# Performance work log

Hardware: AMD Instinct MI355X
Metric: run time of the kernel (lower is better)

Reference implementation:

```python
import jax, jax.numpy as jnp
import numpy as np

N_NODES = 100000
IN_FEATS = 512
H_FEATS = 128
N_HOPS = 3
N_NIE = N_HOPS + 1  # 4 per-hop branches
N_EDGES = 1600000


def _layernorm(z, g, b, eps=1e-5):
    mu = jnp.mean(z, axis=-1, keepdims=True)
    var = jnp.var(z, axis=-1, keepdims=True)
    return (z - mu) * jax.lax.rsqrt(var + eps) * g + b


def _mlp(z, W, b, g, be):
    # Dropout(p=0) -> Linear -> LayerNorm -> ReLU (eval mode)
    return jax.nn.relu(_layernorm(z @ W + b, g, be))


def setup_inputs() -> dict:
    key = jax.random.key(0)
    ks = jax.random.split(key, 16)
    ei = jax.random.randint(ks[0], (2, N_EDGES), 0, N_NODES, dtype=jnp.int64)
    feats = jax.random.normal(ks[1], (N_NODES, IN_FEATS), dtype=jnp.float32)
    s_in = 1.0 / np.sqrt(IN_FEATS)
    s_h = 1.0 / np.sqrt(H_FEATS)
    s_c = 1.0 / np.sqrt(N_NIE * H_FEATS)
    return {
        "edge_index": ei,
        "features": feats,
        # unified input transform (transform_first=True): in_feats -> h_feats
        "W_uni": jax.random.normal(ks[2], (IN_FEATS, H_FEATS), jnp.float32) * s_in,
        "b_uni": jnp.zeros((H_FEATS,), jnp.float32),
        "g_uni": jnp.ones((H_FEATS,), jnp.float32),
        "be_uni": jnp.zeros((H_FEATS,), jnp.float32),
        # per-hop independent embeddings: h_feats -> h_feats, one per hop (stacked)
        "W_ind": jax.random.normal(ks[3], (N_NIE, H_FEATS, H_FEATS), jnp.float32) * s_h,
        "b_ind": jnp.zeros((N_NIE, H_FEATS), jnp.float32),
        "g_ind": jnp.ones((N_NIE, H_FEATS), jnp.float32),
        "be_ind": jnp.zeros((N_NIE, H_FEATS), jnp.float32),
        # relation network (RN='concat'): ndim_fc -> h_feats
        "W_rel": jax.random.normal(ks[4], (N_NIE * H_FEATS, H_FEATS), jnp.float32) * s_c,
        "b_rel": jnp.zeros((H_FEATS,), jnp.float32),
        "g_rel": jnp.ones((H_FEATS,), jnp.float32),
        "be_rel": jnp.zeros((H_FEATS,), jnp.float32),
    }


def reference(edge_index, features, W_uni, b_uni, g_uni, be_uni,
              W_ind, b_ind, g_ind, be_ind, W_rel, b_rel, g_rel, be_rel):
    N = features.shape[0]
    # F.normalize(features, dim=1)  (row_normalized=True)
    x = features / jnp.maximum(
        jnp.linalg.norm(features, axis=1, keepdims=True), 1e-12)

    # preprocess_adj: add self loops, then symmetric normalization D^-1/2 A D^-1/2
    loops = jnp.arange(N, dtype=edge_index.dtype)
    row = jnp.concatenate([edge_index[0], loops])
    col = jnp.concatenate([edge_index[1], loops])
    deg = jax.ops.segment_sum(jnp.ones_like(row, dtype=x.dtype), row,
                              num_segments=N)
    dinv = jnp.where(deg > 0, deg ** -0.5, 0.0)
    w = dinv[row] * dinv[col]  # [E+N] edge weights

    def spmm(z):
        # out[row] += w * z[col]   (gather + scatter-add, memory-bound)
        return jax.ops.segment_sum(w[:, None] * z[col], row, num_segments=N)

    # transform_first: unified embedding before multi-hop aggregation
    h = _mlp(x, W_uni, b_uni, g_uni, be_uni)  # [N, H]

    # inceptive aggregation: hop-0 is h itself, hop-i = A^i h; per-hop MLPs
    z = h
    ns = [_mlp(z, W_ind[0], b_ind[0], g_ind[0], be_ind[0])]
    for i in range(1, N_NIE):
        z = spmm(z)
        ns.append(_mlp(z, W_ind[i], b_ind[i], g_ind[i], be_ind[i]))

    cat = jnp.concatenate(ns, axis=1)  # [N, 4*H]
    out = _mlp(cat, W_rel, b_rel, g_rel, be_rel)  # [N, H]
    return out
```

## Files before the change

kernel.cpp:

```cpp
#include <hip/hip_runtime.h>
#include <hip/hip_bf16.h>

#define NN 100000
#define FE 512
#define HF 128
#define NE 1600000
#define NNIE 4

typedef __attribute__((ext_vector_type(8))) __bf16 bf16x8;
typedef __attribute__((ext_vector_type(4))) float f32x4;
typedef __attribute__((ext_vector_type(8))) unsigned short ushort8;

__device__ __forceinline__ unsigned short f2bf(float f) {
    unsigned u = __float_as_uint(f);
    unsigned r = (u + 0x7fffu + ((u >> 16) & 1u)) >> 16;
    return (unsigned short)r;
}
__device__ __forceinline__ float b2f(unsigned short u) {
    return __uint_as_float(((unsigned)u) << 16);
}

__global__ __launch_bounds__(256) void k_zero(int* __restrict__ deg,
                                              int* __restrict__ cursor, int n) {
    int i = blockIdx.x * 256 + threadIdx.x;
    if (i < n) { deg[i] = 0; cursor[i] = 0; }
}

__global__ __launch_bounds__(256) void k_count(const int* __restrict__ row,
                                               int* __restrict__ deg, int e) {
    int i = blockIdx.x * 256 + threadIdx.x;
    if (i < e) atomicAdd(&deg[row[i]], 1);
}

__global__ __launch_bounds__(256) void k_dinv(const int* __restrict__ deg,
                                              float* __restrict__ dinv, int n) {
    int i = blockIdx.x * 256 + threadIdx.x;
    if (i < n) dinv[i] = 1.0f / sqrtf((float)(deg[i] + 1));
}

__global__ __launch_bounds__(1024) void k_scan1(const int* __restrict__ cnt,
                                                int* __restrict__ off,
                                                int* __restrict__ bsum, int n) {
    __shared__ int wsum[16];
    const int tid = threadIdx.x, lane = tid & 63, wid = tid >> 6;
    const int i = blockIdx.x * 1024 + tid;
    const int v = (i < n) ? cnt[i] : 0;
    int x = v;
#pragma unroll
    for (int s = 1; s < 64; s <<= 1) {
        int t = __shfl_up(x, s);
        if (lane >= s) x += t;
    }
    if (lane == 63) wsum[wid] = x;
    __syncthreads();
    if (wid == 0 && lane < 16) {
        int t = wsum[lane];
#pragma unroll
        for (int s = 1; s < 16; s <<= 1) {
            int u = __shfl_up(t, s);
            if (lane >= s) t += u;
        }
        wsum[lane] = t;
    }
    __syncthreads();
    const int wexc = (wid == 0) ? 0 : wsum[wid - 1];
    if (i < n) off[i] = wexc + x - v;
    if (tid == 0) bsum[blockIdx.x] = wsum[15];
}
__global__ __launch_bounds__(1024) void k_scan2(int* __restrict__ bsum, int nb,
                                                int* __restrict__ total_out) {
    __shared__ int wsum[16];
    const int tid = threadIdx.x, lane = tid & 63, wid = tid >> 6;
    const int v = (tid < nb) ? bsum[tid] : 0;
    int x = v;
#pragma unroll
    for (int s = 1; s < 64; s <<= 1) {
        int t = __shfl_up(x, s);
        if (lane >= s) x += t;
    }
    if (lane == 63) wsum[wid] = x;
    __syncthreads();
    if (wid == 0 && lane < 16) {
        int t = wsum[lane];
#pragma unroll
        for (int s = 1; s < 16; s <<= 1) {
            int u = __shfl_up(t, s);
            if (lane >= s) t += u;
        }
        wsum[lane] = t;
    }
    __syncthreads();
    const int wexc = (wid == 0) ? 0 : wsum[wid - 1];
    if (tid < nb) bsum[tid] = wexc + x - v;
    if (tid == 0) *total_out = wsum[15];
}
__global__ __launch_bounds__(256) void k_scan3(int* __restrict__ off,
                                               const int* __restrict__ bsum,
                                               int n) {
    int i = blockIdx.x * 256 + threadIdx.x;
    if (i < n) off[i] += bsum[i >> 10];
}

__global__ __launch_bounds__(256) void k_fill(const int* __restrict__ rows,
                                              const int* __restrict__ cols,
                                              const float* __restrict__ dinv,
                                              const int* __restrict__ off,
                                              int* __restrict__ cursor,
                                              int* __restrict__ col_s,
                                              float* __restrict__ w_s, int e) {
    int i = blockIdx.x * 256 + threadIdx.x;
    if (i < e) {
        int r = rows[i], c = cols[i];
        int pos = off[r] + atomicAdd(&cursor[r], 1);
        col_s[pos] = c;
        w_s[pos] = dinv[r] * dinv[c];
    }
}

__global__ __launch_bounds__(256) void k_wt(const float* __restrict__ W,
                                            unsigned short* __restrict__ Wt,
                                            int K) {
    int i = blockIdx.x * 256 + threadIdx.x;
    if (i < K * 128) {
        int k = i >> 7, n = i & 127;
        Wt[n * K + k] = f2bf(W[i]);
    }
}

__global__ __launch_bounds__(256) void k_spmm(
    const unsigned short* __restrict__ z, unsigned short* __restrict__ y,
    const int* __restrict__ off, const int* __restrict__ cols,
    const float* __restrict__ w, const float* __restrict__ dinv, int n) {
    const int node = blockIdx.x * 4 + (threadIdx.x >> 6);
    if (node >= n) return;
    const int lane = threadIdx.x & 63;
    const int g = lane >> 4;
    const int l = lane & 15;

    float acc[8];
#pragma unroll
    for (int j = 0; j < 8; j++) acc[j] = 0.0f;

    const int p0 = off[node], p1 = off[node + 1];
    int p = p0 + g;
    for (; p + 4 < p1; p += 8) {
        const int c0 = cols[p], c1 = cols[p + 4];
        const float w0 = w[p], w1 = w[p + 4];
        const ushort8 t0 = *(const ushort8*)(z + (size_t)c0 * HF + 8 * l);
        const ushort8 t1 = *(const ushort8*)(z + (size_t)c1 * HF + 8 * l);
#pragma unroll
        for (int j = 0; j < 8; j++) acc[j] = fmaf(w0, b2f(t0[j]), acc[j]);
#pragma unroll
        for (int j = 0; j < 8; j++) acc[j] = fmaf(w1, b2f(t1[j]), acc[j]);
    }
    if (p < p1) {
        const int c0 = cols[p];
        const float w0 = w[p];
        const ushort8 t0 = *(const ushort8*)(z + (size_t)c0 * HF + 8 * l);
#pragma unroll
        for (int j = 0; j < 8; j++) acc[j] = fmaf(w0, b2f(t0[j]), acc[j]);
    }
    if (g == 0) {
        const float di = dinv[node];
        const ushort8 v = *(const ushort8*)(z + (size_t)node * HF + 8 * l);
        const float d2 = di * di;
#pragma unroll
        for (int j = 0; j < 8; j++) acc[j] = fmaf(d2, b2f(v[j]), acc[j]);
    }
#pragma unroll
    for (int j = 0; j < 8; j++) {
        acc[j] += __shfl_xor(acc[j], 16);
        acc[j] += __shfl_xor(acc[j], 32);
    }
    if (g == 0) {
        ushort8 o;
#pragma unroll
        for (int j = 0; j < 8; j++) o[j] = f2bf(acc[j]);
        *(ushort8*)(y + (size_t)node * HF + 8 * l) = o;
    }
}

template <int K, bool NORM, typename AT, typename OT>
__global__ __launch_bounds__(256) void gemm_mfma(
    const AT* __restrict__ A, int lda, const unsigned short* __restrict__ Wt,
    const float* __restrict__ bias, const float* __restrict__ g,
    const float* __restrict__ be, OT* __restrict__ out, int ldo, int M) {
    constexpr int LDT = 40;
    __shared__ unsigned short Ast[64][LDT];
    __shared__ unsigned short Bst[128][LDT];
    __shared__ float rn_s[64];

    const int tid = threadIdx.x;
    const int row0 = blockIdx.x * 64;
    const int w = tid >> 6;
    const int lane = tid & 63;
    const int m = lane & 15;
    const int q = lane >> 4;
    const int lrow = tid >> 2;
    const int lq = tid & 3;

    f32x4 acc[8];
#pragma unroll
    for (int t = 0; t < 8; t++) acc[t] = (f32x4){0.f, 0.f, 0.f, 0.f};

    float sumsq = 0.0f;
    const bool arow_ok = (row0 + lrow) < M;

    for (int k0 = 0; k0 < K; k0 += 32) {
        __syncthreads();
        ushort8 pk;
        if constexpr (sizeof(AT) == 4) {
            f32x4 a0 = (f32x4){0.f, 0.f, 0.f, 0.f}, a1 = a0;
            if (arow_ok) {
                const float* Ap =
                    (const float*)A + (size_t)(row0 + lrow) * lda + k0 + 8 * lq;
                a0 = *(const f32x4*)Ap;
                a1 = *(const f32x4*)(Ap + 4);
            }
            if (NORM) {
#pragma unroll
                for (int j = 0; j < 4; j++)
                    sumsq += a0[j] * a0[j] + a1[j] * a1[j];
            }
#pragma unroll
            for (int j = 0; j < 4; j++) {
                pk[j] = f2bf(a0[j]);
                pk[j + 4] = f2bf(a1[j]);
            }
        } else {
            pk = (ushort8){0, 0, 0, 0, 0, 0, 0, 0};
            if (arow_ok)
                pk = *(const ushort8*)((const unsigned short*)A +
                                       (size_t)(row0 + lrow) * lda + k0 +
                                       8 * lq);
        }
        *(ushort8*)&Ast[lrow][8 * lq] = pk;
#pragma unroll
        for (int j = 0; j < 2; j++) {
            int c = tid + 256 * j;
            int nn = c >> 2, qq = c & 3;
            ushort8 bchunk =
                *(const ushort8*)(Wt + (size_t)nn * K + k0 + 8 * qq);
            *(ushort8*)&Bst[nn][8 * qq] = bchunk;
        }
        __syncthreads();
        bf16x8 af = *(const bf16x8*)&Ast[16 * w + m][8 * q];
#pragma unroll
        for (int t = 0; t < 8; t++) {
            bf16x8 bfv = *(const bf16x8*)&Bst[16 * t + m][8 * q];
            acc[t] = __builtin_amdgcn_mfma_f32_16x16x32_bf16(af, bfv, acc[t], 0,
                                                             0, 0);
        }
    }

    if (NORM) {
        sumsq += __shfl_xor(sumsq, 1);
        sumsq += __shfl_xor(sumsq, 2);
        if (lq == 0) rn_s[lrow] = 1.0f / fmaxf(sqrtf(sumsq), 1e-12f);
        __syncthreads();
    }

    float bb[8], gg[8], ee[8];
#pragma unroll
    for (int t = 0; t < 8; t++) {
        bb[t] = bias[16 * t + m];
        gg[t] = g[16 * t + m];
        ee[t] = be[16 * t + m];
    }
#pragma unroll
    for (int r = 0; r < 4; r++) {
        const int lrow2 = 16 * w + 4 * q + r;
        float rn = 1.0f;
        if (NORM) rn = rn_s[lrow2];
        float s1 = 0.f, s2 = 0.f;
#pragma unroll
        for (int t = 0; t < 8; t++) {
            float y = fmaf(acc[t][r], rn, bb[t]);
            s1 += y;
            s2 = fmaf(y, y, s2);
        }
#pragma unroll
        for (int mask = 1; mask <= 8; mask <<= 1) {
            s1 += __shfl_xor(s1, mask);
            s2 += __shfl_xor(s2, mask);
        }
        const float mean = s1 * (1.0f / 128.0f);
        const float var = fmaxf(s2 * (1.0f / 128.0f) - mean * mean, 0.0f);
        const float rstd = rsqrtf(var + 1e-5f);
        const int grow = row0 + lrow2;
        if (grow < M) {
#pragma unroll
            for (int t = 0; t < 8; t++) {
                float y = fmaf(acc[t][r], rn, bb[t]);
                float o = fmaxf(fmaf((y - mean) * rstd, gg[t], ee[t]), 0.0f);
                if constexpr (sizeof(OT) == 2)
                    ((unsigned short*)out)[(size_t)grow * ldo + 16 * t + m] =
                        f2bf(o);
                else
                    ((float*)out)[(size_t)grow * ldo + 16 * t + m] = o;
            }
        }
    }
}

extern "C" void kernel_launch(void* const* d_in, const int* in_sizes, int n_in,
                              void* d_out, int out_size, void* d_ws,
                              size_t ws_size, hipStream_t stream) {
    const int* ei = (const int*)d_in[0];
    const float* feats = (const float*)d_in[1];
    const float* W_uni = (const float*)d_in[2];
    const float* b_uni = (const float*)d_in[3];
    const float* g_uni = (const float*)d_in[4];
    const float* be_uni = (const float*)d_in[5];
    const float* W_ind = (const float*)d_in[6];
    const float* b_ind = (const float*)d_in[7];
    const float* g_ind = (const float*)d_in[8];
    const float* be_ind = (const float*)d_in[9];
    const float* W_rel = (const float*)d_in[10];
    const float* b_rel = (const float*)d_in[11];
    const float* g_rel = (const float*)d_in[12];
    const float* be_rel = (const float*)d_in[13];
    float* out = (float*)d_out;

    char* p = (char*)d_ws;
    auto alloc = [&](size_t bytes) {
        void* r = (void*)p;
        p += (bytes + 255) & ~(size_t)255;
        return r;
    };
    int* deg = (int*)alloc(NN * 4);
    int* cursor = (int*)alloc(NN * 4);
    int* off = (int*)alloc((NN + 1) * 4);
    int* bsum = (int*)alloc(1024 * 4);
    int* col_s = (int*)alloc((size_t)NE * 4);
    float* w_s = (float*)alloc((size_t)NE * 4);
    float* dinv = (float*)alloc(NN * 4);
    unsigned short* Wt_uni = (unsigned short*)alloc(128 * FE * 2);
    unsigned short* Wt_rel = (unsigned short*)alloc(128 * (NNIE * HF) * 2);
    unsigned short* Wt_ind = (unsigned short*)alloc(NNIE * HF * HF * 2);
    unsigned short* h = (unsigned short*)alloc((size_t)NN * HF * 2);
    unsigned short* za = (unsigned short*)alloc((size_t)NN * HF * 2);
    unsigned short* zb = (unsigned short*)alloc((size_t)NN * HF * 2);
    unsigned short* cat = (unsigned short*)alloc((size_t)NN * NNIE * HF * 2);

    const int gE = (NE + 255) / 256;
    const int gN = (NN + 255) / 256;
    const int gGemm = (NN + 63) / 64;
    const int gSpmm = (NN + 3) / 4;
    const int nbScan = (NN + 1023) / 1024;
    const int* erow = ei;
    const int* ecol = ei + NE;

    k_zero<<<gN, 256, 0, stream>>>(deg, cursor, NN);
    k_count<<<gE, 256, 0, stream>>>(erow, deg, NE);
    k_dinv<<<gN, 256, 0, stream>>>(deg, dinv, NN);
    k_scan1<<<nbScan, 1024, 0, stream>>>(deg, off, bsum, NN);
    k_scan2<<<1, 1024, 0, stream>>>(bsum, nbScan, off + NN);
    k_scan3<<<gN, 256, 0, stream>>>(off, bsum, NN);
    k_fill<<<gE, 256, 0, stream>>>(erow, ecol, dinv, off, cursor, col_s, w_s,
                                   NE);

    k_wt<<<(FE * 128 + 255) / 256, 256, 0, stream>>>(W_uni, Wt_uni, FE);
    k_wt<<<(NNIE * HF * 128 + 255) / 256, 256, 0, stream>>>(W_rel, Wt_rel,
                                                            NNIE * HF);
    for (int hh = 0; hh < NNIE; hh++)
        k_wt<<<(HF * 128 + 255) / 256, 256, 0, stream>>>(
            W_ind + hh * HF * HF, Wt_ind + hh * HF * HF, HF);

    gemm_mfma<FE, true, float, unsigned short>
        <<<gGemm, 256, 0, stream>>>(feats, FE, Wt_uni, b_uni, g_uni, be_uni, h,
                                    HF, NN);
    gemm_mfma<HF, false, unsigned short, unsigned short>
        <<<gGemm, 256, 0, stream>>>(h, HF, Wt_ind + 0 * HF * HF, b_ind, g_ind,
                                    be_ind, cat + 0 * HF, NNIE * HF, NN);
    k_spmm<<<gSpmm, 256, 0, stream>>>(h, za, off, col_s, w_s, dinv, NN);
    gemm_mfma<HF, false, unsigned short, unsigned short>
        <<<gGemm, 256, 0, stream>>>(za, HF, Wt_ind + 1 * HF * HF, b_ind + HF,
                                    g_ind + HF, be_ind + HF, cat + 1 * HF,
                                    NNIE * HF, NN);
    k_spmm<<<gSpmm, 256, 0, stream>>>(za, zb, off, col_s, w_s, dinv, NN);
    gemm_mfma<HF, false, unsigned short, unsigned short>
        <<<gGemm, 256, 0, stream>>>(zb, HF, Wt_ind + 2 * HF * HF,
                                    b_ind + 2 * HF, g_ind + 2 * HF,
                                    be_ind + 2 * HF, cat + 2 * HF, NNIE * HF,
                                    NN);
    k_spmm<<<gSpmm, 256, 0, stream>>>(zb, za, off, col_s, w_s, dinv, NN);
    gemm_mfma<HF, false, unsigned short, unsigned short>
        <<<gGemm, 256, 0, stream>>>(za, HF, Wt_ind + 3 * HF * HF,
                                    b_ind + 3 * HF, g_ind + 3 * HF,
                                    be_ind + 3 * HF, cat + 3 * HF, NNIE * HF,
                                    NN);
    gemm_mfma<NNIE * HF, false, unsigned short, float>
        <<<gGemm, 256, 0, stream>>>(cat, NNIE * HF, Wt_rel, b_rel, g_rel,
                                    be_rel, out, HF, NN);
}
```

Measured before the change: 822.5 us.

## Pack edge col/weight, unroll SpMM, widen GEMM K-tile, merge setup kernels

Stores each CSR edge's column and weight together as an int2, so SpMM issues one 8-byte load per edge instead of two separate streams. SpMM's inner loop is unrolled to four outstanding gathers. The generic MFMA GEMM now stages 64-wide K tiles per sync instead of 32, and a dedicated K=128 GEMM loads the whole tile once with a single barrier. It also folds dinv into the scan kernel and merges the six weight-transpose launches into one, trading more LDS per block and more registers for fewer launches and barriers.

```diff
diff --git a/kernel.cpp b/kernel.cpp
--- a/kernel.cpp
+++ b/kernel.cpp
@@ -32,19 +32,16 @@
     if (i < e) atomicAdd(&deg[row[i]], 1);
 }
 
-__global__ __launch_bounds__(256) void k_dinv(const int* __restrict__ deg,
-                                              float* __restrict__ dinv, int n) {
-    int i = blockIdx.x * 256 + threadIdx.x;
-    if (i < n) dinv[i] = 1.0f / sqrtf((float)(deg[i] + 1));
-}
-
 __global__ __launch_bounds__(1024) void k_scan1(const int* __restrict__ cnt,
                                                 int* __restrict__ off,
-                                                int* __restrict__ bsum, int n) {
+                                                int* __restrict__ bsum,
+                                                float* __restrict__ dinv,
+                                                int n) {
     __shared__ int wsum[16];
     const int tid = threadIdx.x, lane = tid & 63, wid = tid >> 6;
     const int i = blockIdx.x * 1024 + tid;
     const int v = (i < n) ? cnt[i] : 0;
+    if (i < n) dinv[i] = rsqrtf((float)(v + 1));
     int x = v;
 #pragma unroll
     for (int s = 1; s < 64; s <<= 1) {
@@ -106,31 +103,39 @@
                                               const float* __restrict__ dinv,
                                               const int* __restrict__ off,
                                               int* __restrict__ cursor,
-                                              int* __restrict__ col_s,
-                                              float* __restrict__ w_s, int e) {
+                                              int2* __restrict__ es, int e) {
     int i = blockIdx.x * 256 + threadIdx.x;
     if (i < e) {
         int r = rows[i], c = cols[i];
         int pos = off[r] + atomicAdd(&cursor[r], 1);
-        col_s[pos] = c;
-        w_s[pos] = dinv[r] * dinv[c];
-    }
-}
-
-__global__ __launch_bounds__(256) void k_wt(const float* __restrict__ W,
-                                            unsigned short* __restrict__ Wt,
-                                            int K) {
+        es[pos] = make_int2(c, __float_as_int(dinv[r] * dinv[c]));
+    }
+}
+
+__global__ __launch_bounds__(256) void k_wt_all(
+    const float* __restrict__ Wu, const float* __restrict__ Wr,
+    const float* __restrict__ Wi, unsigned short* __restrict__ Tu,
+    unsigned short* __restrict__ Tr, unsigned short* __restrict__ Ti) {
     int i = blockIdx.x * 256 + threadIdx.x;
-    if (i < K * 128) {
+    if (i < 65536) {
         int k = i >> 7, n = i & 127;
-        Wt[n * K + k] = f2bf(W[i]);
+        Tu[n * 512 + k] = f2bf(Wu[i]);
+    } else if (i < 131072) {
+        int j = i - 65536;
+        int k = j >> 7, n = j & 127;
+        Tr[n * 512 + k] = f2bf(Wr[j]);
+    } else if (i < 196608) {
+        int j = i - 131072;
+        int hh = j >> 14, r = j & 16383;
+        int k = r >> 7, n = r & 127;
+        Ti[hh * 16384 + n * 128 + k] = f2bf(Wi[j]);
     }
 }
 
 __global__ __launch_bounds__(256) void k_spmm(
     const unsigned short* __restrict__ z, unsigned short* __restrict__ y,
-    const int* __restrict__ off, const int* __restrict__ cols,
-    const float* __restrict__ w, const float* __restrict__ dinv, int n) {
+    const int* __restrict__ off, const int2* __restrict__ es,
+    const float* __restrict__ dinv, int n) {
     const int node = blockIdx.x * 4 + (threadIdx.x >> 6);
     if (node >= n) return;
     const int lane = threadIdx.x & 63;
@@ -143,20 +148,37 @@
 
     const int p0 = off[node], p1 = off[node + 1];
     int p = p0 + g;
+    for (; p + 12 < p1; p += 16) {
+        const int2 e0 = es[p], e1 = es[p + 4], e2 = es[p + 8], e3 = es[p + 12];
+        const ushort8 t0 = *(const ushort8*)(z + (size_t)e0.x * HF + 8 * l);
+        const ushort8 t1 = *(const ushort8*)(z + (size_t)e1.x * HF + 8 * l);
+        const ushort8 t2 = *(const ushort8*)(z + (size_t)e2.x * HF + 8 * l);
+        const ushort8 t3 = *(const ushort8*)(z + (size_t)e3.x * HF + 8 * l);
+        const float w0 = __int_as_float(e0.y), w1 = __int_as_float(e1.y);
+        const float w2 = __int_as_float(e2.y), w3 = __int_as_float(e3.y);
+#pragma unroll
+        for (int j = 0; j < 8; j++) acc[j] = fmaf(w0, b2f(t0[j]), acc[j]);
+#pragma unroll
+        for (int j = 0; j < 8; j++) acc[j] = fmaf(w1, b2f(t1[j]), acc[j]);
+#pragma unroll
+        for (int j = 0; j < 8; j++) acc[j] = fmaf(w2, b2f(t2[j]), acc[j]);
+#pragma unroll
+        for (int j = 0; j < 8; j++) acc[j] = fmaf(w3, b2f(t3[j]), acc[j]);
+    }
     for (; p + 4 < p1; p += 8) {
-        const int c0 = cols[p], c1 = cols[p + 4];
-        const float w0 = w[p], w1 = w[p + 4];
-        const ushort8 t0 = *(const ushort8*)(z + (size_t)c0 * HF + 8 * l);
-        const ushort8 t1 = *(const ushort8*)(z + (size_t)c1 * HF + 8 * l);
+        const int2 e0 = es[p], e1 = es[p + 4];
+        const ushort8 t0 = *(const ushort8*)(z + (size_t)e0.x * HF + 8 * l);
+        const ushort8 t1 = *(const ushort8*)(z + (size_t)e1.x * HF + 8 * l);
+        const float w0 = __int_as_float(e0.y), w1 = __int_as_float(e1.y);
 #pragma unroll
         for (int j = 0; j < 8; j++) acc[j] = fmaf(w0, b2f(t0[j]), acc[j]);
 #pragma unroll
         for (int j = 0; j < 8; j++) acc[j] = fmaf(w1, b2f(t1[j]), acc[j]);
     }
     if (p < p1) {
-        const int c0 = cols[p];
-        const float w0 = w[p];
-        const ushort8 t0 = *(const ushort8*)(z + (size_t)c0 * HF + 8 * l);
+        const int2 e0 = es[p];
+        const ushort8 t0 = *(const ushort8*)(z + (size_t)e0.x * HF + 8 * l);
+        const float w0 = __int_as_float(e0.y);
 #pragma unroll
         for (int j = 0; j < 8; j++) acc[j] = fmaf(w0, b2f(t0[j]), acc[j]);
     }
@@ -185,7 +207,7 @@
     const AT* __restrict__ A, int lda, const unsigned short* __restrict__ Wt,
     const float* __restrict__ bias, const float* __restrict__ g,
     const float* __restrict__ be, OT* __restrict__ out, int ldo, int M) {
-    constexpr int LDT = 40;
+    constexpr int LDT = 72;
     __shared__ unsigned short Ast[64][LDT];
     __shared__ unsigned short Bst[128][LDT];
     __shared__ float rn_s[64];
@@ -206,50 +228,57 @@
     float sumsq = 0.0f;
     const bool arow_ok = (row0 + lrow) < M;
 
-    for (int k0 = 0; k0 < K; k0 += 32) {
+    for (int k0 = 0; k0 < K; k0 += 64) {
         __syncthreads();
-        ushort8 pk;
-        if constexpr (sizeof(AT) == 4) {
-            f32x4 a0 = (f32x4){0.f, 0.f, 0.f, 0.f}, a1 = a0;
-            if (arow_ok) {
-                const float* Ap =
-                    (const float*)A + (size_t)(row0 + lrow) * lda + k0 + 8 * lq;
-                a0 = *(const f32x4*)Ap;
-                a1 = *(const f32x4*)(Ap + 4);
+#pragma unroll
+        for (int oo = 0; oo < 2; oo++) {
+            const int o = lq + 4 * oo;
+            ushort8 pk;
+            if constexpr (sizeof(AT) == 4) {
+                f32x4 a0 = (f32x4){0.f, 0.f, 0.f, 0.f}, a1 = a0;
+                if (arow_ok) {
+                    const float* Ap = (const float*)A +
+                                      (size_t)(row0 + lrow) * lda + k0 + 8 * o;
+                    a0 = *(const f32x4*)Ap;
+                    a1 = *(const f32x4*)(Ap + 4);
+                }
+                if (NORM) {
+#pragma unroll
+                    for (int j = 0; j < 4; j++)
+                        sumsq += a0[j] * a0[j] + a1[j] * a1[j];
+                }
+#pragma unroll
+                for (int j = 0; j < 4; j++) {
+                    pk[j] = f2bf(a0[j]);
+                    pk[j + 4] = f2bf(a1[j]);
+                }
+            } else {
+                pk = (ushort8){0, 0, 0, 0, 0, 0, 0, 0};
+                if (arow_ok)
+                    pk = *(const ushort8*)((const unsigned short*)A +
+                                           (size_t)(row0 + lrow) * lda + k0 +
+                                           8 * o);
             }
-            if (NORM) {
-#pragma unroll
-                for (int j = 0; j < 4; j++)
-                    sumsq += a0[j] * a0[j] + a1[j] * a1[j];
+            *(ushort8*)&Ast[lrow][8 * o] = pk;
+        }
+        const int bn = tid >> 1;
+#pragma unroll
+        for (int kk = 0; kk < 4; kk++) {
+            const int o = (tid & 1) + 2 * kk;
+            *(ushort8*)&Bst[bn][8 * o] =
+                *(const ushort8*)(Wt + (size_t)bn * K + k0 + 8 * o);
+        }
+        __syncthreads();
+#pragma unroll
+        for (int jj = 0; jj < 2; jj++) {
+            bf16x8 af = *(const bf16x8*)&Ast[16 * w + m][8 * q + 32 * jj];
+#pragma unroll
+            for (int t = 0; t < 8; t++) {
+                bf16x8 bfv = *(const bf16x8*)&Bst[16 * t + m][8 * q + 32 * jj];
+                acc[t] = __builtin_amdgcn_mfma_f32_16x16x32_bf16(af, bfv,
+                                                                 acc[t], 0, 0,
+                                                                 0);
             }
-#pragma unroll
-            for (int j = 0; j < 4; j++) {
-                pk[j] = f2bf(a0[j]);
-                pk[j + 4] = f2bf(a1[j]);
-            }
-        } else {
-            pk = (ushort8){0, 0, 0, 0, 0, 0, 0, 0};
-            if (arow_ok)
-                pk = *(const ushort8*)((const unsigned short*)A +
-                                       (size_t)(row0 + lrow) * lda + k0 +
-                                       8 * lq);
-        }
-        *(ushort8*)&Ast[lrow][8 * lq] = pk;
-#pragma unroll
-        for (int j = 0; j < 2; j++) {
-            int c = tid + 256 * j;
-            int nn = c >> 2, qq = c & 3;
-            ushort8 bchunk =
-                *(const ushort8*)(Wt + (size_t)nn * K + k0 + 8 * qq);
-            *(ushort8*)&Bst[nn][8 * qq] = bchunk;
-        }
-        __syncthreads();
-        bf16x8 af = *(const bf16x8*)&Ast[16 * w + m][8 * q];
-#pragma unroll
-        for (int t = 0; t < 8; t++) {
-            bf16x8 bfv = *(const bf16x8*)&Bst[16 * t + m][8 * q];
-            acc[t] = __builtin_amdgcn_mfma_f32_16x16x32_bf16(af, bfv, acc[t], 0,
-                                                             0, 0);
         }
     }
 
@@ -298,6 +327,93 @@
                         f2bf(o);
                 else
                     ((float*)out)[(size_t)grow * ldo + 16 * t + m] = o;
+            }
+        }
+    }
+}
+
+__global__ __launch_bounds__(256) void gemm128(
+    const unsigned short* __restrict__ A,
+    const unsigned short* __restrict__ Wt, const float* __restrict__ bias,
+    const float* __restrict__ g, const float* __restrict__ be,
+    unsigned short* __restrict__ out, int ldo, int M) {
+    constexpr int LDT = 136;
+    __shared__ unsigned short Ast[64][LDT];
+    __shared__ unsigned short Bst[128][LDT];
+
+    const int tid = threadIdx.x;
+    const int row0 = blockIdx.x * 64;
+    const int w = tid >> 6;
+    const int lane = tid & 63;
+    const int m = lane & 15;
+    const int q = lane >> 4;
+    const int lrow = tid >> 2;
+    const int lq = tid & 3;
+
+    const bool arow_ok = (row0 + lrow) < M;
+#pragma unroll
+    for (int k = 0; k < 4; k++) {
+        const int o = lq + 4 * k;
+        ushort8 pk = (ushort8){0, 0, 0, 0, 0, 0, 0, 0};
+        if (arow_ok)
+            pk = *(const ushort8*)(A + (size_t)(row0 + lrow) * HF + 8 * o);
+        *(ushort8*)&Ast[lrow][8 * o] = pk;
+    }
+    const int bn = tid >> 1;
+#pragma unroll
+    for (int k = 0; k < 8; k++) {
+        const int o = (tid & 1) + 2 * k;
+        *(ushort8*)&Bst[bn][8 * o] =
+            *(const ushort8*)(Wt + (size_t)bn * HF + 8 * o);
+    }
+    __syncthreads();
+
+    f32x4 acc[8];
+#pragma unroll
+    for (int t = 0; t < 8; t++) acc[t] = (f32x4){0.f, 0.f, 0.f, 0.f};
+#pragma unroll
+    for (int jj = 0; jj < 4; jj++) {
+        bf16x8 af = *(const bf16x8*)&Ast[16 * w + m][8 * q + 32 * jj];
+#pragma unroll
+        for (int t = 0; t < 8; t++) {
+            bf16x8 bfv = *(const bf16x8*)&Bst[16 * t + m][8 * q + 32 * jj];
+            acc[t] = __builtin_amdgcn_mfma_f32_16x16x32_bf16(af, bfv, acc[t], 0,
+                                                             0, 0);
+        }
+    }
+
+    float bb[8], gg[8], ee[8];
+#pragma unroll
+    for (int t = 0; t < 8; t++) {
+        bb[t] = bias[16 * t + m];
+        gg[t] = g[16 * t + m];
+        ee[t] = be[16 * t + m];
+    }
+#pragma unroll
+    for (int r = 0; r < 4; r++) {
+        const int lrow2 = 16 * w + 4 * q + r;
+        float s1 = 0.f, s2 = 0.f;
+#pragma unroll
+        for (int t = 0; t < 8; t++) {
+            float y = acc[t][r] + bb[t];
+            s1 += y;
+            s2 = fmaf(y, y, s2);
+        }
+#pragma unroll
+        for (int mask = 1; mask <= 8; mask <<= 1) {
+            s1 += __shfl_xor(s1, mask);
+            s2 += __shfl_xor(s2, mask);
+        }
+        const float mean = s1 * (1.0f / 128.0f);
+        const float var = fmaxf(s2 * (1.0f / 128.0f) - mean * mean, 0.0f);
+        const float rstd = rsqrtf(var + 1e-5f);
+        const int grow = row0 + lrow2;
+        if (grow < M) {
+#pragma unroll
+            for (int t = 0; t < 8; t++) {
+                float y = acc[t][r] + bb[t];
+                float o = fmaxf(fmaf((y - mean) * rstd, gg[t], ee[t]), 0.0f);
+                out[(size_t)grow * ldo + 16 * t + m] = f2bf(o);
             }
         }
     }
@@ -332,8 +448,7 @@
     int* cursor = (int*)alloc(NN * 4);
     int* off = (int*)alloc((NN + 1) * 4);
     int* bsum = (int*)alloc(1024 * 4);
-    int* col_s = (int*)alloc((size_t)NE * 4);
-    float* w_s = (float*)alloc((size_t)NE * 4);
+    int2* es = (int2*)alloc((size_t)NE * 8);
     float* dinv = (float*)alloc(NN * 4);
     unsigned short* Wt_uni = (unsigned short*)alloc(128 * FE * 2);
     unsigned short* Wt_rel = (unsigned short*)alloc(128 * (NNIE * HF) * 2);
@@ -353,43 +468,33 @@
 
     k_zero<<<gN, 256, 0, stream>>>(deg, cursor, NN);
     k_count<<<gE, 256, 0, stream>>>(erow, deg, NE);
-    k_dinv<<<gN, 256, 0, stream>>>(deg, dinv, NN);
-    k_scan1<<<nbScan, 1024, 0, stream>>>(deg, off, bsum, NN);
+    k_scan1<<<nbScan, 1024, 0, stream>>>(deg, off, bsum, dinv, NN);
     k_scan2<<<1, 1024, 0, stream>>>(bsum, nbScan, off + NN);
     k_scan3<<<gN, 256, 0, stream>>>(off, bsum, NN);
-    k_fill<<<gE, 256, 0, stream>>>(erow, ecol, dinv, off, cursor, col_s, w_s,
-                                   NE);
-
-    k_wt<<<(FE * 128 + 255) / 256, 256, 0, stream>>>(W_uni, Wt_uni, FE);
-    k_wt<<<(NNIE * HF * 128 + 255) / 256, 256, 0, stream>>>(W_rel, Wt_rel,
-                                                            NNIE * HF);
-    for (int hh = 0; hh < NNIE; hh++)
-        k_wt<<<(HF * 128 + 255) / 256, 256, 0, stream>>>(
-            W_ind + hh * HF * HF, Wt_ind + hh * HF * HF, HF);
+    k_fill<<<gE, 256, 0, stream>>>(erow, ecol, dinv, off, cursor, es, NE);
+
+    k_wt_all<<<(196608 + 255) / 256, 256, 0, stream>>>(W_uni, W_rel, W_ind,
+                                                       Wt_uni, Wt_rel, Wt_ind);
 
     gemm_mfma<FE, true, float, unsigned short>
         <<<gGemm, 256, 0, stream>>>(feats, FE, Wt_uni, b_uni, g_uni, be_uni, h,
                                     HF, NN);
-    gemm_mfma<HF, false, unsigned short, unsigned short>
-        <<<gGemm, 256, 0, stream>>>(h, HF, Wt_ind + 0 * HF * HF, b_ind, g_ind,
-                                    be_ind, cat + 0 * HF, NNIE * HF, NN);
-    k_spmm<<<gSpmm, 256, 0, stream>>>(h, za, off, col_s, w_s, dinv, NN);
-    gemm_mfma<HF, false, unsigned short, unsigned short>
-        <<<gGemm, 256, 0, stream>>>(za, HF, Wt_ind + 1 * HF * HF, b_ind + HF,
-                                    g_ind + HF, be_ind + HF, cat + 1 * HF,
-                                    NNIE * HF, NN);
-    k_spmm<<<gSpmm, 256, 0, stream>>>(za, zb, off, col_s, w_s, dinv, NN);
-    gemm_mfma<HF, false, unsigned short, unsigned short>
-        <<<gGemm, 256, 0, stream>>>(zb, HF, Wt_ind + 2 * HF * HF,
-                                    b_ind + 2 * HF, g_ind + 2 * HF,
-                                    be_ind + 2 * HF, cat + 2 * HF, NNIE * HF,
-                                    NN);
-    k_spmm<<<gSpmm, 256, 0, stream>>>(zb, za, off, col_s, w_s, dinv, NN);
-    gemm_mfma<HF, false, unsigned short, unsigned short>
-        <<<gGemm, 256, 0, stream>>>(za, HF, Wt_ind + 3 * HF * HF,
-                                    b_ind + 3 * HF, g_ind + 3 * HF,
-                                    be_ind + 3 * HF, cat + 3 * HF, NNIE * HF,
-                                    NN);
+    gemm128<<<gGemm, 256, 0, stream>>>(h, Wt_ind + 0 * HF * HF, b_ind, g_ind,
+                                       be_ind, cat + 0 * HF, NNIE * HF, NN);
+    k_spmm<<<gSpmm, 256, 0, stream>>>(h, za, off, es, dinv, NN);
+    gemm128<<<gGemm, 256, 0, stream>>>(za, Wt_ind + 1 * HF * HF, b_ind + HF,
+                                       g_ind + HF, be_ind + HF, cat + 1 * HF,
+                                       NNIE * HF, NN);
+    k_spmm<<<gSpmm, 256, 0, stream>>>(za, zb, off, es, dinv, NN);
+    gemm128<<<gGemm, 256, 0, stream>>>(zb, Wt_ind + 2 * HF * HF,
+                                       b_ind + 2 * HF, g_ind + 2 * HF,
+                                       be_ind + 2 * HF, cat + 2 * HF,
+                                       NNIE * HF, NN);
+    k_spmm<<<gSpmm, 256, 0, stream>>>(zb, za, off, es, dinv, NN);
+    gemm128<<<gGemm, 256, 0, stream>>>(za, Wt_ind + 3 * HF * HF,
+                                       b_ind + 3 * HF, g_ind + 3 * HF,
+                                       be_ind + 3 * HF, cat + 3 * HF,
+                                       NNIE * HF, NN);
     gemm_mfma<NNIE * HF, false, unsigned short, float>
         <<<gGemm, 256, 0, stream>>>(cat, NNIE * HF, Wt_rel, b_rel, g_rel,
                                     be_rel, out, HF, NN);
```

Result: faster. 791.2 us (-3.8%).
